# Kernel optimization log

Measured on AMD Instinct MI355X. Metric: run time of the kernel, lower is better.

## Reference

```python
import jax, jax.numpy as jnp
import numpy as np

NEG_BIG = 1e10


def setup_inputs() -> dict:
    key = jax.random.key(0)
    k1, k2 = jax.random.split(key)
    B, S, D = 8, 2048, 64
    T = 2048  # static tgt_max (stands in for tgt_lens.max())
    src_tok_features = jax.random.normal(k1, (B, S, D), dtype=jnp.float32)
    src_mask = jnp.ones((B, S), dtype=jnp.float32)
    lengthscale = jnp.array(1.0, dtype=jnp.float32)
    # lengths in [T//2, T] so tgt_lens != src_lens (skip identity branch) and no div-by-zero
    tgt_lens = jax.random.randint(k2, (B,), T // 2, T + 1, dtype=jnp.int32)
    return {
        "src_tok_features": src_tok_features,
        "src_mask": src_mask,
        "lengthscale": lengthscale,
        "tgt_lens": tgt_lens,
        "tgt_max": T,
    }


def reference(src_tok_features, src_mask, lengthscale, tgt_lens, tgt_max):
    # src_tok_features: (B, S, D); src_mask: (B, S) float; tgt_lens: (B,) int
    B, S, D = src_tok_features.shape
    T = int(tgt_max)
    src_lens = src_mask.sum(-1)                      # (B,)
    tl = tgt_lens.astype(src_lens.dtype)             # (B,)
    len_ratio = src_lens / tl                        # (B,)

    src_idx = jnp.arange(S, dtype=jnp.float32)       # (S,)
    tgt_idx = jnp.arange(T, dtype=jnp.float32)       # (T,)
    # (B, S, T): squared distance between src position and scaled tgt position
    sq_diff = (src_idx[None, :, None] - len_ratio[:, None, None] * tgt_idx[None, None, :]) ** 2
    logits = -sq_diff / (2.0 * lengthscale ** 2)
    m = src_mask[..., None]                          # (B, S, 1)
    logits = m * logits - (1.0 - m) * NEG_BIG
    weights = jax.nn.softmax(logits, axis=-2)        # normalize over src tokens
    # weighted sum over src dim without materializing (B, S, T, D)
    tgt_tok_features = jnp.einsum('bst,bsd->btd', weights, src_tok_features)
    tgt_mask = tgt_idx[None, :] < tl[:, None]        # (B, T) bool
    return tgt_tok_features, tgt_mask
```

## Files before the change

### kernel.cpp

```cpp
#include <hip/hip_runtime.h>
#include <hip/hip_bf16.h>

#define NEG_BIG 1e10f

__global__ void prep_ratios(const float* __restrict__ mask,
                            const int* __restrict__ tgt_lens,
                            float* __restrict__ ratios, int S) {
    int b = blockIdx.x;
    float s = 0.f;
    for (int i = threadIdx.x; i < S; i += blockDim.x)
        s += mask[(size_t)b * S + i];
    for (int off = 32; off > 0; off >>= 1)
        s += __shfl_xor(s, off, 64);
    __shared__ float ws[8];
    int wid = threadIdx.x >> 6;
    int lane = threadIdx.x & 63;
    if (lane == 0) ws[wid] = s;
    __syncthreads();
    if (threadIdx.x == 0) {
        float tot = 0.f;
        int nw = blockDim.x >> 6;
        for (int i = 0; i < nw; i++) tot += ws[i];
        ratios[b] = tot / (float)tgt_lens[b];
    }
}

constexpr int TPW = 4;
constexpr int NROWS = 80;

__global__ void __launch_bounds__(256)
length_transform(const float* __restrict__ x,
                 const float* __restrict__ mask,
                 const float* __restrict__ lengthscale,
                 const int* __restrict__ tgt_lens,
                 const float* __restrict__ ratios,
                 float* __restrict__ out_feat,
                 float* __restrict__ out_mask,
                 int B, int S, int T) {
    __shared__ float4 wlds_all[4][NROWS];
    const int wid  = threadIdx.x >> 6;
    const int lane = threadIdx.x & 63;
    const int nt = T / TPW;
    int gw = blockIdx.x * 4 + wid;
    const bool active = (gw < B * nt);
    if (!active) gw = 0;
    const int b  = gw / nt;
    const int t0 = (gw - b * nt) * TPW;

    const float ls = lengthscale[0];
    const float fac = 1.0f / (2.0f * ls * ls);
    const float r = ratios[b];

    int su[TPW]; float c[TPW];
#pragma unroll
    for (int i = 0; i < TPW; ++i) {
        c[i] = r * (float)(t0 + i);
        int s0 = (int)rintf(c[i]) - 32;
        if (s0 < 0) s0 = 0;
        if (s0 > S - 64) s0 = S - 64;
        su[i] = s0;
    }
    int u0 = su[0];
    if (u0 > S - NROWS) u0 = S - NROWS;
    if (u0 < 0) u0 = 0;
#pragma unroll
    for (int i = 0; i < TPW; ++i) {
        int hi = u0 + (NROWS - 64);
        su[i] = su[i] > hi ? hi : (su[i] < u0 ? u0 : su[i]);
    }

    float4* wlds = wlds_all[wid];
    for (int i = lane; i < NROWS; i += 64)
        wlds[i] = make_float4(0.f, 0.f, 0.f, 0.f);
    __syncthreads();

#pragma unroll
    for (int i = 0; i < TPW; ++i) {
        int s = su[i] + lane;
        float dsv = (float)s - c[i];
        float mv = mask[(size_t)b * S + s];
        float logit = mv * (-dsv * dsv * fac) - (1.0f - mv) * NEG_BIG;
        int sstar = (int)rintf(c[i]);
        if (sstar < su[i]) sstar = su[i];
        if (sstar > su[i] + 63) sstar = su[i] + 63;
        float dstar = (float)sstar - c[i];
        float mx = -dstar * dstar * fac;
        float w = expf(logit - mx);
        float dn = w;
        for (int off = 32; off > 0; off >>= 1)
            dn += __shfl_xor(dn, off, 64);
        w *= 1.0f / fmaxf(dn, 1e-30f);
        ((float*)&wlds[s - u0])[i] = w;
    }
    __syncthreads();

    const int g = lane >> 4;
    const int cidx = (lane & 15) << 2;
    const float* xp = x + ((size_t)b * S + (size_t)(u0 + g)) * 64 + cidx;
    float4 a0 = {0,0,0,0}, a1 = {0,0,0,0}, a2 = {0,0,0,0}, a3 = {0,0,0,0};
#pragma unroll 5
    for (int j = 0; j < NROWS / 4; ++j) {
        float4 v  = *(const float4*)(xp + (size_t)(4 * j) * 64);
        float4 wv = wlds[4 * j + g];
        a0.x = fmaf(wv.x, v.x, a0.x); a0.y = fmaf(wv.x, v.y, a0.y);
        a0.z = fmaf(wv.x, v.z, a0.z); a0.w = fmaf(wv.x, v.w, a0.w);
        a1.x = fmaf(wv.y, v.x, a1.x); a1.y = fmaf(wv.y, v.y, a1.y);
        a1.z = fmaf(wv.y, v.z, a1.z); a1.w = fmaf(wv.y, v.w, a1.w);
        a2.x = fmaf(wv.z, v.x, a2.x); a2.y = fmaf(wv.z, v.y, a2.y);
        a2.z = fmaf(wv.z, v.z, a2.z); a2.w = fmaf(wv.z, v.w, a2.w);
        a3.x = fmaf(wv.w, v.x, a3.x); a3.y = fmaf(wv.w, v.y, a3.y);
        a3.z = fmaf(wv.w, v.z, a3.z); a3.w = fmaf(wv.w, v.w, a3.w);
    }

#pragma unroll
    for (int off = 16; off <= 32; off <<= 1) {
        a0.x += __shfl_xor(a0.x, off, 64); a0.y += __shfl_xor(a0.y, off, 64);
        a0.z += __shfl_xor(a0.z, off, 64); a0.w += __shfl_xor(a0.w, off, 64);
        a1.x += __shfl_xor(a1.x, off, 64); a1.y += __shfl_xor(a1.y, off, 64);
        a1.z += __shfl_xor(a1.z, off, 64); a1.w += __shfl_xor(a1.w, off, 64);
        a2.x += __shfl_xor(a2.x, off, 64); a2.y += __shfl_xor(a2.y, off, 64);
        a2.z += __shfl_xor(a2.z, off, 64); a2.w += __shfl_xor(a2.w, off, 64);
        a3.x += __shfl_xor(a3.x, off, 64); a3.y += __shfl_xor(a3.y, off, 64);
        a3.z += __shfl_xor(a3.z, off, 64); a3.w += __shfl_xor(a3.w, off, 64);
    }

    if (active) {
        float4 myacc = a0;
        if (g == 1) myacc = a1;
        else if (g == 2) myacc = a2;
        else if (g == 3) myacc = a3;
        *(float4*)(out_feat + ((size_t)b * T + (size_t)(t0 + g)) * 64 + cidx) = myacc;
        if (lane < TPW)
            out_mask[(size_t)b * T + t0 + lane] = (t0 + lane < tgt_lens[b]) ? 1.0f : 0.0f;
    }
}

extern "C" void kernel_launch(void* const* d_in, const int* in_sizes, int n_in,
                              void* d_out, int out_size, void* d_ws, size_t ws_size,
                              hipStream_t stream) {
    const float* x        = (const float*)d_in[0];
    const float* mask     = (const float*)d_in[1];
    const float* ls       = (const float*)d_in[2];
    const int*   tgt_lens = (const int*)d_in[3];

    int B = in_sizes[3];
    int S = in_sizes[1] / B;
    int D = in_sizes[0] / (B * S);
    int T = out_size / (B * (D + 1));

    float* ratios = (float*)d_ws;
    float* out_feat = (float*)d_out;
    float* out_mask = out_feat + (size_t)B * T * D;

    prep_ratios<<<B, 256, 0, stream>>>(mask, tgt_lens, ratios, S);

    int waves = B * (T / TPW);
    int grid = (waves + 3) / 4;
    length_transform<<<grid, 256, 0, stream>>>(x, mask, ls, tgt_lens, ratios,
                                               out_feat, out_mask, B, S, T);
}
```

Before: 72.71 us.

## Fuse ratio prep into main kernel, double targets per wave, drop block barriers

Removes the separate prep_ratios launch: each wave now sums the mask row itself with float4 loads and a wave reduction. Targets per wave go from 4 to 8, so each loaded feature row feeds twice as many accumulators and the grid halves. The weight tile in LDS is widened to two float4 per row. The __syncthreads calls are dropped because each wave uses only its own LDS slice. The trade-offs are redundant mask reads in every wave, which L2 should largely absorb, and more accumulator registers.

```diff
diff --git a/kernel.cpp b/kernel.cpp
--- a/kernel.cpp
+++ b/kernel.cpp
@@ -3,29 +3,7 @@
 
 #define NEG_BIG 1e10f
 
-__global__ void prep_ratios(const float* __restrict__ mask,
-                            const int* __restrict__ tgt_lens,
-                            float* __restrict__ ratios, int S) {
-    int b = blockIdx.x;
-    float s = 0.f;
-    for (int i = threadIdx.x; i < S; i += blockDim.x)
-        s += mask[(size_t)b * S + i];
-    for (int off = 32; off > 0; off >>= 1)
-        s += __shfl_xor(s, off, 64);
-    __shared__ float ws[8];
-    int wid = threadIdx.x >> 6;
-    int lane = threadIdx.x & 63;
-    if (lane == 0) ws[wid] = s;
-    __syncthreads();
-    if (threadIdx.x == 0) {
-        float tot = 0.f;
-        int nw = blockDim.x >> 6;
-        for (int i = 0; i < nw; i++) tot += ws[i];
-        ratios[b] = tot / (float)tgt_lens[b];
-    }
-}
-
-constexpr int TPW = 4;
+constexpr int TPW = 8;
 constexpr int NROWS = 80;
 
 __global__ void __launch_bounds__(256)
@@ -33,11 +11,10 @@
                  const float* __restrict__ mask,
                  const float* __restrict__ lengthscale,
                  const int* __restrict__ tgt_lens,
-                 const float* __restrict__ ratios,
                  float* __restrict__ out_feat,
                  float* __restrict__ out_mask,
                  int B, int S, int T) {
-    __shared__ float4 wlds_all[4][NROWS];
+    __shared__ float4 wlds_all[4][NROWS][2];
     const int wid  = threadIdx.x >> 6;
     const int lane = threadIdx.x & 63;
     const int nt = T / TPW;
@@ -47,9 +24,23 @@
     const int b  = gw / nt;
     const int t0 = (gw - b * nt) * TPW;
 
+    float msum = 0.f;
+    {
+        const float4* m4 = (const float4*)(mask + (size_t)b * S);
+        const int n4 = S >> 2;
+        for (int i = lane; i < n4; i += 64) {
+            float4 v = m4[i];
+            msum += v.x + v.y + v.z + v.w;
+        }
+        for (int i = (n4 << 2) + lane; i < S; i += 64)
+            msum += mask[(size_t)b * S + i];
+        for (int off = 32; off > 0; off >>= 1)
+            msum += __shfl_xor(msum, off, 64);
+    }
+    const float r = msum / (float)tgt_lens[b];
+
     const float ls = lengthscale[0];
     const float fac = 1.0f / (2.0f * ls * ls);
-    const float r = ratios[b];
 
     int su[TPW]; float c[TPW];
 #pragma unroll
@@ -69,10 +60,15 @@
         su[i] = su[i] > hi ? hi : (su[i] < u0 ? u0 : su[i]);
     }
 
-    float4* wlds = wlds_all[wid];
-    for (int i = lane; i < NROWS; i += 64)
-        wlds[i] = make_float4(0.f, 0.f, 0.f, 0.f);
-    __syncthreads();
+    float4 (*wlds)[2] = wlds_all[wid];
+    {
+        float4* wf = &wlds[0][0];
+#pragma unroll
+        for (int i = 0; i < (NROWS * 2 + 63) / 64; ++i) {
+            int k = i * 64 + lane;
+            if (k < NROWS * 2) wf[k] = make_float4(0.f, 0.f, 0.f, 0.f);
+        }
+    }
 
 #pragma unroll
     for (int i = 0; i < TPW; ++i) {
@@ -90,46 +86,55 @@
         for (int off = 32; off > 0; off >>= 1)
             dn += __shfl_xor(dn, off, 64);
         w *= 1.0f / fmaxf(dn, 1e-30f);
-        ((float*)&wlds[s - u0])[i] = w;
+        ((float*)&wlds[s - u0][i >> 2])[i & 3] = w;
     }
-    __syncthreads();
 
     const int g = lane >> 4;
     const int cidx = (lane & 15) << 2;
     const float* xp = x + ((size_t)b * S + (size_t)(u0 + g)) * 64 + cidx;
-    float4 a0 = {0,0,0,0}, a1 = {0,0,0,0}, a2 = {0,0,0,0}, a3 = {0,0,0,0};
+    float4 a[TPW];
+#pragma unroll
+    for (int i = 0; i < TPW; ++i) a[i] = make_float4(0.f, 0.f, 0.f, 0.f);
 #pragma unroll 5
     for (int j = 0; j < NROWS / 4; ++j) {
-        float4 v  = *(const float4*)(xp + (size_t)(4 * j) * 64);
-        float4 wv = wlds[4 * j + g];
-        a0.x = fmaf(wv.x, v.x, a0.x); a0.y = fmaf(wv.x, v.y, a0.y);
-        a0.z = fmaf(wv.x, v.z, a0.z); a0.w = fmaf(wv.x, v.w, a0.w);
-        a1.x = fmaf(wv.y, v.x, a1.x); a1.y = fmaf(wv.y, v.y, a1.y);
-        a1.z = fmaf(wv.y, v.z, a1.z); a1.w = fmaf(wv.y, v.w, a1.w);
-        a2.x = fmaf(wv.z, v.x, a2.x); a2.y = fmaf(wv.z, v.y, a2.y);
-        a2.z = fmaf(wv.z, v.z, a2.z); a2.w = fmaf(wv.z, v.w, a2.w);
-        a3.x = fmaf(wv.w, v.x, a3.x); a3.y = fmaf(wv.w, v.y, a3.y);
-        a3.z = fmaf(wv.w, v.z, a3.z); a3.w = fmaf(wv.w, v.w, a3.w);
+        float4 v   = *(const float4*)(xp + (size_t)(4 * j) * 64);
+        float4 wlo = wlds[4 * j + g][0];
+        float4 whi = wlds[4 * j + g][1];
+        a[0].x = fmaf(wlo.x, v.x, a[0].x); a[0].y = fmaf(wlo.x, v.y, a[0].y);
+        a[0].z = fmaf(wlo.x, v.z, a[0].z); a[0].w = fmaf(wlo.x, v.w, a[0].w);
+        a[1].x = fmaf(wlo.y, v.x, a[1].x); a[1].y = fmaf(wlo.y, v.y, a[1].y);
+        a[1].z = fmaf(wlo.y, v.z, a[1].z); a[1].w = fmaf(wlo.y, v.w, a[1].w);
+        a[2].x = fmaf(wlo.z, v.x, a[2].x); a[2].y = fmaf(wlo.z, v.y, a[2].y);
+        a[2].z = fmaf(wlo.z, v.z, a[2].z); a[2].w = fmaf(wlo.z, v.w, a[2].w);
+        a[3].x = fmaf(wlo.w, v.x, a[3].x); a[3].y = fmaf(wlo.w, v.y, a[3].y);
+        a[3].z = fmaf(wlo.w, v.z, a[3].z); a[3].w = fmaf(wlo.w, v.w, a[3].w);
+        a[4].x = fmaf(whi.x, v.x, a[4].x); a[4].y = fmaf(whi.x, v.y, a[4].y);
+        a[4].z = fmaf(whi.x, v.z, a[4].z); a[4].w = fmaf(whi.x, v.w, a[4].w);
+        a[5].x = fmaf(whi.y, v.x, a[5].x); a[5].y = fmaf(whi.y, v.y, a[5].y);
+        a[5].z = fmaf(whi.y, v.z, a[5].z); a[5].w = fmaf(whi.y, v.w, a[5].w);
+        a[6].x = fmaf(whi.z, v.x, a[6].x); a[6].y = fmaf(whi.z, v.y, a[6].y);
+        a[6].z = fmaf(whi.z, v.z, a[6].z); a[6].w = fmaf(whi.z, v.w, a[6].w);
+        a[7].x = fmaf(whi.w, v.x, a[7].x); a[7].y = fmaf(whi.w, v.y, a[7].y);
+        a[7].z = fmaf(whi.w, v.z, a[7].z); a[7].w = fmaf(whi.w, v.w, a[7].w);
     }
 
 #pragma unroll
     for (int off = 16; off <= 32; off <<= 1) {
-        a0.x += __shfl_xor(a0.x, off, 64); a0.y += __shfl_xor(a0.y, off, 64);
-        a0.z += __shfl_xor(a0.z, off, 64); a0.w += __shfl_xor(a0.w, off, 64);
-        a1.x += __shfl_xor(a1.x, off, 64); a1.y += __shfl_xor(a1.y, off, 64);
-        a1.z += __shfl_xor(a1.z, off, 64); a1.w += __shfl_xor(a1.w, off, 64);
-        a2.x += __shfl_xor(a2.x, off, 64); a2.y += __shfl_xor(a2.y, off, 64);
-        a2.z += __shfl_xor(a2.z, off, 64); a2.w += __shfl_xor(a2.w, off, 64);
-        a3.x += __shfl_xor(a3.x, off, 64); a3.y += __shfl_xor(a3.y, off, 64);
-        a3.z += __shfl_xor(a3.z, off, 64); a3.w += __shfl_xor(a3.w, off, 64);
+#pragma unroll
+        for (int i = 0; i < TPW; ++i) {
+            a[i].x += __shfl_xor(a[i].x, off, 64);
+            a[i].y += __shfl_xor(a[i].y, off, 64);
+            a[i].z += __shfl_xor(a[i].z, off, 64);
+            a[i].w += __shfl_xor(a[i].w, off, 64);
+        }
     }
 
     if (active) {
-        float4 myacc = a0;
-        if (g == 1) myacc = a1;
-        else if (g == 2) myacc = a2;
-        else if (g == 3) myacc = a3;
-        *(float4*)(out_feat + ((size_t)b * T + (size_t)(t0 + g)) * 64 + cidx) = myacc;
+        float4 s_lo = (g == 0) ? a[0] : (g == 1) ? a[1] : (g == 2) ? a[2] : a[3];
+        float4 s_hi = (g == 0) ? a[4] : (g == 1) ? a[5] : (g == 2) ? a[6] : a[7];
+        float* orow = out_feat + ((size_t)b * T + (size_t)(t0 + g)) * 64 + cidx;
+        *(float4*)orow = s_lo;
+        *(float4*)(orow + (size_t)4 * 64) = s_hi;
         if (lane < TPW)
             out_mask[(size_t)b * T + t0 + lane] = (t0 + lane < tgt_lens[b]) ? 1.0f : 0.0f;
     }
@@ -148,14 +153,11 @@
     int D = in_sizes[0] / (B * S);
     int T = out_size / (B * (D + 1));
 
-    float* ratios = (float*)d_ws;
     float* out_feat = (float*)d_out;
     float* out_mask = out_feat + (size_t)B * T * D;
 
-    prep_ratios<<<B, 256, 0, stream>>>(mask, tgt_lens, ratios, S);
-
     int waves = B * (T / TPW);
     int grid = (waves + 3) / 4;
-    length_transform<<<grid, 256, 0, stream>>>(x, mask, ls, tgt_lens, ratios,
+    length_transform<<<grid, 256, 0, stream>>>(x, mask, ls, tgt_lens,
                                                out_feat, out_mask, B, S, T);
 }
```

After: 77.01 us. +5.9%, slower.
